# Optimization experiments

Measured on AMD Instinct MI355X. Metric: run time of the kernel, lower is better.

The kernel has to match this reference:

```python
import jax, jax.numpy as jnp
import numpy as np

N, D, E = 16384, 2048, 64   # tokens, d_model, num_experts
K = 9                        # self.k = min(k+1, num_experts) with k=8
EPS = 0.01
SIGMA = 1.0 / E              # Normal(0, 1/num_experts) stddev


def setup_inputs() -> dict:
    key = jax.random.key(0)
    ks = jax.random.split(key, 6)
    x = jax.random.normal(ks[0], (N, D), jnp.float32)
    Wr = jax.random.normal(ks[1], (D, E), jnp.float32) * 0.02
    br = jnp.zeros((E,), jnp.float32)
    Wn = jax.random.normal(ks[2], (D, E), jnp.float32) * 0.02
    bn = jnp.zeros((E,), jnp.float32)
    noise_eps = jax.random.normal(ks[3], (N, E), jnp.float32)
    # torch: (-empty.exponential_()).log() -> log of Exp(1) samples
    gumbel_noise = jnp.log(jax.random.exponential(ks[4], (N, E), jnp.float32))
    return {"x": x, "Wr": Wr, "br": br, "Wn": Wn, "bn": bn,
            "noise_eps": noise_eps, "gumbel_noise": gumbel_noise}


def reference(x, Wr, br, Wn, bn, noise_eps, gumbel_noise):
    raw_logits = x @ Wr + br                              # [N, E]
    noise_stddev = jax.nn.softplus(x @ Wn + bn) + EPS     # [N, E]
    noisy_logits = raw_logits + noise_eps * noise_stddev  # [N, E]

    top_vals, top_idx = jax.lax.top_k(noisy_logits, K)    # [N, K] sorted desc
    # scatter ones at top-k indices (indices unique per row)
    hard_mask = jax.nn.one_hot(top_idx, E, dtype=noisy_logits.dtype).sum(axis=1)  # [N, E]

    # gumbel-softmax straight-through relaxation
    mask_soft = jax.nn.softmax(noisy_logits + gumbel_noise, axis=-1)
    expert_mask = hard_mask - jax.lax.stop_gradient(mask_soft) + mask_soft

    route_prob = jax.nn.softmax(noisy_logits, axis=-1)    # [N, E]
    importance = jax.nn.softmax(raw_logits, axis=-1).sum(axis=0)  # [E]

    # load: P(raw + noise > threshold), Normal(0, 1/E) CDF per original
    threshold = top_vals[:, K - 1]                        # [N]
    z = (threshold[:, None] - raw_logits) / noise_stddev  # [N, E]
    cdf = 0.5 * (1.0 + jax.scipy.special.erf(z / (SIGMA * jnp.sqrt(jnp.float32(2.0)))))
    load = (1.0 - cdf).sum(axis=0)                        # [E]

    return (expert_mask, route_prob, importance, load)
```

## Files before the change

### kernel.cpp

```cpp
#include <hip/hip_runtime.h>
#include <hip/hip_bf16.h>
#include <math.h>

#define N_TOK 16384
#define DIM   2048
#define NE    64
#define TOPK  9

#define ROWS     16
#define DC       64
#define NCHUNK   (DIM / DC)
#define NTHREADS 256
#define NBUF     4

typedef short  short8  __attribute__((ext_vector_type(8)));
typedef float  float4_ __attribute__((ext_vector_type(4)));
typedef unsigned short ushort_t;

__device__ __forceinline__ void async16(const void* g, void* l) {
    __builtin_amdgcn_global_load_lds(
        (const __attribute__((address_space(1))) void*)g,
        (__attribute__((address_space(3))) void*)l, 16, 0, 0);
}

__device__ __forceinline__ unsigned pk2(float a, float b) {
    float2 f; f.x = a; f.y = b;
    __hip_bfloat162 h = __float22bfloat162_rn(f);
    unsigned u;
    __builtin_memcpy(&u, &h, 4);
    return u;
}

__device__ __forceinline__ void cvt8(const float4_ va, const float4_ vb,
                                     short8* h, short8* l) {
    union { short8 s; unsigned u[4]; } H, L;
    const float f[8] = {va[0], va[1], va[2], va[3], vb[0], vb[1], vb[2], vb[3]};
#pragma unroll
    for (int i = 0; i < 4; ++i) {
        const float a = f[2 * i], b = f[2 * i + 1];
        const unsigned p = pk2(a, b);
        H.u[i] = p;
        const float ha = __uint_as_float(p << 16);
        const float hb = __uint_as_float(p & 0xffff0000u);
        L.u[i] = pk2(a - ha, b - hb);
    }
    *h = H.s; *l = L.s;
}

__device__ __forceinline__ void wave_max64_2(float& a, float& b) {
#pragma unroll
    for (int off = 32; off > 0; off >>= 1) {
        const float ax = __shfl_xor(a, off, 64);
        const float bx = __shfl_xor(b, off, 64);
        a = fmaxf(a, ax);
        b = fmaxf(b, bx);
    }
}

__device__ __forceinline__ void wave_sum64_3(float& a, float& b, float& c) {
#pragma unroll
    for (int off = 32; off > 0; off >>= 1) {
        const float ax = __shfl_xor(a, off, 64);
        const float bx = __shfl_xor(b, off, 64);
        const float cx = __shfl_xor(c, off, 64);
        a += ax;
        b += bx;
        c += cx;
    }
}

__global__ __launch_bounds__(256)
void prep_w(const float* __restrict__ Wr, const float* __restrict__ Wn,
            ushort_t* __restrict__ wsW)
{
    const int gid = blockIdx.x * 256 + threadIdx.x;
    const int l   = gid & 63;
    const int ct  = (gid >> 6) & 7;
    const int kcg = gid >> 9;
    const int n   = ct * 16 + (l & 15);
    const int k0  = kcg * 32 + (l >> 4) * 8;
    const float* src = (n < NE) ? (Wr + n) : (Wn + (n - NE));
    union { short8 s; ushort_t us[8]; } H, L;
#pragma unroll
    for (int j = 0; j < 8; ++j) {
        const float v = src[(size_t)(k0 + j) * NE];
        const unsigned uv = __float_as_uint(v);
        const unsigned hb = (uv + 0x7fffu + ((uv >> 16) & 1u)) & 0xffff0000u;
        const float lo = v - __uint_as_float(hb);
        const unsigned ul = __float_as_uint(lo);
        H.us[j] = (ushort_t)(hb >> 16);
        L.us[j] = (ushort_t)((ul + 0x7fffu + ((ul >> 16) & 1u)) >> 16);
    }
    const size_t s0 = (size_t)(kcg * 8 + ct) * 2;
    *(short8*)(wsW + s0 * 512 + l * 8)         = H.s;
    *(short8*)(wsW + (s0 + 1) * 512 + l * 8)   = L.s;
}

struct BFrag { short8 h[2][2]; short8 l[2][2]; };

__device__ __forceinline__ void load_b(const char* __restrict__ wsB,
                                       int ch, int w, int lane, BFrag& b) {
#pragma unroll
    for (int kc = 0; kc < 2; ++kc)
#pragma unroll
        for (int cc = 0; cc < 2; ++cc) {
            const size_t off = (size_t)(((ch * 2 + kc) * 8) + 2 * w + cc) * 2048
                             + (size_t)lane * 16;
            b.h[kc][cc] = *(const short8*)(wsB + off);
            b.l[kc][cc] = *(const short8*)(wsB + off + 1024);
        }
}

__device__ __forceinline__ void mfma_chunk(const float* __restrict__ xb,
                                           const int (&aoff)[2][2],
                                           const BFrag& b,
                                           float4_ (&acc)[2]) {
#pragma unroll
    for (int kc = 0; kc < 2; ++kc) {
        const float4_ va = *(const float4_*)(xb + aoff[kc][0]);
        const float4_ vb = *(const float4_*)(xb + aoff[kc][1]);
        short8 ah, al;
        cvt8(va, vb, &ah, &al);
#pragma unroll
        for (int cc = 0; cc < 2; ++cc) {
            acc[cc] = __builtin_amdgcn_mfma_f32_16x16x32_bf16(ah, b.h[kc][cc], acc[cc], 0, 0, 0);
            acc[cc] = __builtin_amdgcn_mfma_f32_16x16x32_bf16(al, b.h[kc][cc], acc[cc], 0, 0, 0);
            acc[cc] = __builtin_amdgcn_mfma_f32_16x16x32_bf16(ah, b.l[kc][cc], acc[cc], 0, 0, 0);
        }
    }
}

__global__ __launch_bounds__(NTHREADS, 4)
void moe_main(const float* __restrict__ x,
              const float* __restrict__ br,
              const float* __restrict__ bn,
              const float* __restrict__ noise_eps,
              const float* __restrict__ gumbel,
              const ushort_t* __restrict__ wsW,
              float* __restrict__ out)
{
    __shared__ __align__(16) float smem[4352];

    const int t    = threadIdx.x;
    const int lane = t & 63;
    const int w    = t >> 6;
    const int c4   = lane & 15;
    const int q    = lane >> 4;
    const int row0 = blockIdx.x * ROWS;

    const int  srow = 4 * w + q;
    const int  sgk  = c4 ^ (srow & 15);
    const float* gxb = x + (size_t)(row0 + srow) * DIM + sgk * 4;
    const int  lxo  = w * 256;

    int aoff[2][2];
#pragma unroll
    for (int kc = 0; kc < 2; ++kc) {
        const int g0 = kc * 8 + q * 2;
        aoff[kc][0] = c4 * 64 + ((g0 ^ c4) * 4);
        aoff[kc][1] = c4 * 64 + (((g0 + 1) ^ c4) * 4);
    }

    float4_ acc[2];
    acc[0] = (float4_)(0.f);
    acc[1] = (float4_)(0.f);

    const char* wsB = (const char*)wsW;

#pragma unroll
    for (int p = 0; p < NBUF - 1; ++p)
        async16(gxb + p * DC, &smem[p * 1024 + lxo]);

    BFrag bA, bB;
    load_b(wsB, 0, w, lane, bA);

#pragma unroll 1
    for (int i = 0; i < NCHUNK - 4; i += 2) {
        asm volatile("s_waitcnt vmcnt(10)" ::: "memory");
        __builtin_amdgcn_s_barrier();
        asm volatile("" ::: "memory");
        load_b(wsB, i + 1, w, lane, bB);
        async16(gxb + (i + 3) * DC, &smem[((i + 3) & 3) * 1024 + lxo]);
        __builtin_amdgcn_sched_barrier(0);
        mfma_chunk(&smem[(i & 3) * 1024], aoff, bA, acc);

        asm volatile("s_waitcnt vmcnt(10)" ::: "memory");
        __builtin_amdgcn_s_barrier();
        asm volatile("" ::: "memory");
        load_b(wsB, i + 2, w, lane, bA);
        async16(gxb + (i + 4) * DC, &smem[((i + 4) & 3) * 1024 + lxo]);
        __builtin_amdgcn_sched_barrier(0);
        mfma_chunk(&smem[((i + 1) & 3) * 1024], aoff, bB, acc);
    }

    asm volatile("s_waitcnt vmcnt(10)" ::: "memory");
    __builtin_amdgcn_s_barrier();
    asm volatile("" ::: "memory");
    load_b(wsB, 29, w, lane, bB);
    async16(gxb + 31 * DC, &smem[3 * 1024 + lxo]);
    __builtin_amdgcn_sched_barrier(0);
    mfma_chunk(&smem[0 * 1024], aoff, bA, acc);

    asm volatile("s_waitcnt vmcnt(10)" ::: "memory");
    __builtin_amdgcn_s_barrier();
    asm volatile("" ::: "memory");
    load_b(wsB, 30, w, lane, bA);
    __builtin_amdgcn_sched_barrier(0);
    mfma_chunk(&smem[1 * 1024], aoff, bB, acc);

    asm volatile("s_waitcnt vmcnt(9)" ::: "memory");
    __builtin_amdgcn_s_barrier();
    asm volatile("" ::: "memory");
    load_b(wsB, 31, w, lane, bB);
    __builtin_amdgcn_sched_barrier(0);
    mfma_chunk(&smem[2 * 1024], aoff, bA, acc);

    asm volatile("s_waitcnt vmcnt(8)" ::: "memory");
    __builtin_amdgcn_s_barrier();
    asm volatile("" ::: "memory");
    __builtin_amdgcn_sched_barrier(0);
    mfma_chunk(&smem[3 * 1024], aoff, bB, acc);

    float epsv[4], gumv[4];
#pragma unroll
    for (int r = 0; r < 4; ++r) {
        const int row = row0 + w * 4 + r;
        epsv[r] = noise_eps[(size_t)row * NE + lane];
        gumv[r] = gumbel  [(size_t)row * NE + lane];
    }

    __syncthreads();
    float* rawS = &smem[0];
    float* noiS = &smem[2080];
#pragma unroll
    for (int cc = 0; cc < 2; ++cc) {
        const int colg = (2 * w + cc) * 16 + c4;
        float* basep = (colg < NE) ? rawS : noiS;
        const int col = colg & 63;
#pragma unroll
        for (int v = 0; v < 4; ++v) {
            const int row = q * 4 + v;
            basep[row * 65 + col] = acc[cc][v];
        }
    }
    __syncthreads();

    const float br_l = br[lane];
    const float bn_l = bn[lane];

    float imp_acc = 0.f, load_acc = 0.f;
    float* out_em   = out;
    float* out_rp   = out + (size_t)N_TOK * NE;
    float* out_imp  = out + (size_t)2 * N_TOK * NE;
    float* out_load = out_imp + NE;

#pragma unroll 1
    for (int r = 0; r < 4; ++r) {
        const int lrow = w * 4 + r;
        const int row  = row0 + lrow;
        const float raw = rawS[lrow * 65 + lane] + br_l;
        const float nl  = noiS[lrow * 65 + lane] + bn_l;
        const float sd = fmaxf(nl, 0.f) + log1pf(expf(-fabsf(nl))) + 0.01f;
        const float noisy = fmaf(epsv[r], sd, raw);

        const unsigned uk  = __float_as_uint(noisy);
        const unsigned key = uk ^ ((uk & 0x80000000u) ? 0xFFFFFFFFu : 0x80000000u);
        unsigned res = 0;
#pragma unroll
        for (int bit = 31; bit >= 0; --bit) {
            const unsigned cand = res | (1u << bit);
            const int cnt = __popcll(__ballot(key >= cand));
            if (cnt >= TOPK) res = cand;
        }
        const float thr  = __uint_as_float(res ^ ((res & 0x80000000u) ? 0x80000000u : 0xFFFFFFFFu));
        const float hard = (key >= res) ? 1.f : 0.f;

        const float g = noisy + gumv[r];
        float mg = g, mr = raw;
        wave_max64_2(mg, mr);

        const float eg = expf(g - mg);
        const float en = expf(noisy - thr);
        const float er = expf(raw - mr);
        float sg = eg, sn = en, sr = er;
        wave_sum64_3(sg, sn, sr);

        const float ms = eg / sg;
        const float em = (hard - ms) + ms;
        const float rp = en / sn;
        imp_acc += er / sr;

        const float z = (thr - raw) / sd;
        load_acc += 0.5f * erfcf(z * 45.254833995939045f);

        out_em[(size_t)row * NE + lane] = em;
        out_rp[(size_t)row * NE + lane] = rp;
    }

    __syncthreads();
    smem[w * 64 + lane]       = imp_acc;
    smem[256 + w * 64 + lane] = load_acc;
    __syncthreads();
    if (w == 0) {
        const float s1 = smem[lane] + smem[64 + lane] + smem[128 + lane] + smem[192 + lane];
        const float s2 = smem[256 + lane] + smem[320 + lane] + smem[384 + lane] + smem[448 + lane];
        atomicAdd(&out_imp[lane], s1);
        atomicAdd(&out_load[lane], s2);
    }
}

extern "C" void kernel_launch(void* const* d_in, const int* in_sizes, int n_in,
                              void* d_out, int out_size, void* d_ws, size_t ws_size,
                              hipStream_t stream)
{
    const float* x         = (const float*)d_in[0];
    const float* Wr        = (const float*)d_in[1];
    const float* br        = (const float*)d_in[2];
    const float* Wn        = (const float*)d_in[3];
    const float* bn        = (const float*)d_in[4];
    const float* noise_eps = (const float*)d_in[5];
    const float* gumbel    = (const float*)d_in[6];
    float* out = (float*)d_out;
    ushort_t* wsW = (ushort_t*)d_ws;

    (void)hipMemsetAsync((char*)d_out + (size_t)2 * N_TOK * NE * sizeof(float), 0,
                         2 * NE * sizeof(float), stream);
    prep_w<<<128, 256, 0, stream>>>(Wr, Wn, wsW);
    moe_main<<<N_TOK / ROWS, NTHREADS, 0, stream>>>(
        x, br, bn, noise_eps, gumbel, wsW, out);
}
```

Before: 261.2 us.

## Restructure GEMM main loop into uniform pipelined steps with 8 LDS buffers

The prologue, steady-state loop and epilogue of the x-tile pipeline are replaced by a templated step that issues the next weight-fragment loads and the async x load before waiting and computing. LDS reads now go through inline-asm ds_read_b128 with an explicit lgkmcnt wait. The LDS ring grows from 4 to 8 buffers and vmcnt thresholds are raised, so more global loads can be in flight before the barrier. Tail steps clamp the chunk indices and issue redundant loads instead of having a special epilogue. The larger shared-memory footprint could reduce occupancy, and the extra tail loads add some memory traffic.

```diff
diff --git a/kernel.cpp b/kernel.cpp
--- a/kernel.cpp
+++ b/kernel.cpp
@@ -11,7 +11,7 @@
 #define DC       64
 #define NCHUNK   (DIM / DC)
 #define NTHREADS 256
-#define NBUF     4
+#define NBUF     8
 
 typedef short  short8  __attribute__((ext_vector_type(8)));
 typedef float  float4_ __attribute__((ext_vector_type(4)));
@@ -21,6 +21,12 @@
     __builtin_amdgcn_global_load_lds(
         (const __attribute__((address_space(1))) void*)g,
         (__attribute__((address_space(3))) void*)l, 16, 0, 0);
+}
+
+__device__ __forceinline__ float4_ ds_read128(unsigned addr) {
+    float4_ d;
+    asm volatile("ds_read_b128 %0, %1" : "=v"(d) : "v"(addr));
+    return d;
 }
 
 __device__ __forceinline__ unsigned pk2(float a, float b) {
@@ -111,23 +117,58 @@
         }
 }
 
-__device__ __forceinline__ void mfma_chunk(const float* __restrict__ xb,
-                                           const int (&aoff)[2][2],
-                                           const BFrag& b,
-                                           float4_ (&acc)[2]) {
-#pragma unroll
-    for (int kc = 0; kc < 2; ++kc) {
-        const float4_ va = *(const float4_*)(xb + aoff[kc][0]);
-        const float4_ vb = *(const float4_*)(xb + aoff[kc][1]);
-        short8 ah, al;
-        cvt8(va, vb, &ah, &al);
-#pragma unroll
-        for (int cc = 0; cc < 2; ++cc) {
-            acc[cc] = __builtin_amdgcn_mfma_f32_16x16x32_bf16(ah, b.h[kc][cc], acc[cc], 0, 0, 0);
-            acc[cc] = __builtin_amdgcn_mfma_f32_16x16x32_bf16(al, b.h[kc][cc], acc[cc], 0, 0, 0);
-            acc[cc] = __builtin_amdgcn_mfma_f32_16x16x32_bf16(ah, b.l[kc][cc], acc[cc], 0, 0, 0);
-        }
-    }
+template<int W>
+__device__ __forceinline__ void wait_vm() {
+    static_assert(W == 11 || W == 19 || W == 27, "unexpected wait");
+    if constexpr (W == 11)      asm volatile("s_waitcnt vmcnt(11)" ::: "memory");
+    else if constexpr (W == 19) asm volatile("s_waitcnt vmcnt(19)" ::: "memory");
+    else                        asm volatile("s_waitcnt vmcnt(27)" ::: "memory");
+}
+
+__device__ __forceinline__ void compute_chunk(unsigned ldsb,
+                                              const unsigned (&aoffB)[2][2],
+                                              const BFrag& b,
+                                              float4_ (&acc)[2]) {
+    const float4_ va0 = ds_read128(ldsb + aoffB[0][0]);
+    const float4_ vb0 = ds_read128(ldsb + aoffB[0][1]);
+    const float4_ va1 = ds_read128(ldsb + aoffB[1][0]);
+    const float4_ vb1 = ds_read128(ldsb + aoffB[1][1]);
+    asm volatile("s_waitcnt lgkmcnt(0)" ::: "memory");
+    __builtin_amdgcn_sched_barrier(0);
+    short8 ah0, al0, ah1, al1;
+    cvt8(va0, vb0, &ah0, &al0);
+    cvt8(va1, vb1, &ah1, &al1);
+#pragma unroll
+    for (int cc = 0; cc < 2; ++cc) {
+        acc[cc] = __builtin_amdgcn_mfma_f32_16x16x32_bf16(ah0, b.h[0][cc], acc[cc], 0, 0, 0);
+        acc[cc] = __builtin_amdgcn_mfma_f32_16x16x32_bf16(al0, b.h[0][cc], acc[cc], 0, 0, 0);
+        acc[cc] = __builtin_amdgcn_mfma_f32_16x16x32_bf16(ah0, b.l[0][cc], acc[cc], 0, 0, 0);
+    }
+#pragma unroll
+    for (int cc = 0; cc < 2; ++cc) {
+        acc[cc] = __builtin_amdgcn_mfma_f32_16x16x32_bf16(ah1, b.h[1][cc], acc[cc], 0, 0, 0);
+        acc[cc] = __builtin_amdgcn_mfma_f32_16x16x32_bf16(al1, b.h[1][cc], acc[cc], 0, 0, 0);
+        acc[cc] = __builtin_amdgcn_mfma_f32_16x16x32_bf16(ah1, b.l[1][cc], acc[cc], 0, 0, 0);
+    }
+}
+
+template<int W>
+__device__ __forceinline__ void step(int i, const char* wsB, int w, int lane,
+                                     BFrag& bload, const BFrag& buse,
+                                     const float* gxb, float* smem, int lxo,
+                                     unsigned ldsbase, const unsigned (&aoffB)[2][2],
+                                     float4_ (&acc)[2])
+{
+    const int bch = (i + 1 < NCHUNK) ? i + 1 : NCHUNK - 1;
+    load_b(wsB, bch, w, lane, bload);
+    __builtin_amdgcn_sched_barrier(0);
+    const int sch = (i + 3 < NCHUNK) ? i + 3 : NCHUNK - 1;
+    async16(gxb + sch * DC, &smem[((i + 3) & (NBUF - 1)) * 1024 + lxo]);
+    __builtin_amdgcn_sched_barrier(0);
+    wait_vm<W>();
+    __builtin_amdgcn_s_barrier();
+    __builtin_amdgcn_sched_barrier(0);
+    compute_chunk(ldsbase + (unsigned)((i & (NBUF - 1)) * 4096), aoffB, buse, acc);
 }
 
 __global__ __launch_bounds__(NTHREADS, 4)
@@ -139,7 +180,7 @@
               const ushort_t* __restrict__ wsW,
               float* __restrict__ out)
 {
-    __shared__ __align__(16) float smem[4352];
+    __shared__ __align__(16) float smem[NBUF * 1024];
 
     const int t    = threadIdx.x;
     const int lane = t & 63;
@@ -153,13 +194,15 @@
     const float* gxb = x + (size_t)(row0 + srow) * DIM + sgk * 4;
     const int  lxo  = w * 256;
 
-    int aoff[2][2];
+    unsigned aoffB[2][2];
 #pragma unroll
     for (int kc = 0; kc < 2; ++kc) {
         const int g0 = kc * 8 + q * 2;
-        aoff[kc][0] = c4 * 64 + ((g0 ^ c4) * 4);
-        aoff[kc][1] = c4 * 64 + (((g0 + 1) ^ c4) * 4);
-    }
+        aoffB[kc][0] = (unsigned)((c4 * 64 + ((g0 ^ c4) * 4)) * 4);
+        aoffB[kc][1] = (unsigned)((c4 * 64 + (((g0 + 1) ^ c4) * 4)) * 4);
+    }
+    const unsigned ldsbase =
+        (unsigned)(unsigned long long)(__attribute__((address_space(3))) void*)(void*)smem;
 
     float4_ acc[2];
     acc[0] = (float4_)(0.f);
@@ -167,59 +210,23 @@
 
     const char* wsB = (const char*)wsW;
 
-#pragma unroll
-    for (int p = 0; p < NBUF - 1; ++p)
-        async16(gxb + p * DC, &smem[p * 1024 + lxo]);
-
     BFrag bA, bB;
     load_b(wsB, 0, w, lane, bA);
-
+    __builtin_amdgcn_sched_barrier(0);
+    async16(gxb + 0 * DC, &smem[0 * 1024 + lxo]);
+    __builtin_amdgcn_sched_barrier(0);
+    async16(gxb + 1 * DC, &smem[1 * 1024 + lxo]);
+    __builtin_amdgcn_sched_barrier(0);
+    async16(gxb + 2 * DC, &smem[2 * 1024 + lxo]);
+    __builtin_amdgcn_sched_barrier(0);
+
+    step<11>(0, wsB, w, lane, bB, bA, gxb, smem, lxo, ldsbase, aoffB, acc);
+    step<19>(1, wsB, w, lane, bA, bB, gxb, smem, lxo, ldsbase, aoffB, acc);
 #pragma unroll 1
-    for (int i = 0; i < NCHUNK - 4; i += 2) {
-        asm volatile("s_waitcnt vmcnt(10)" ::: "memory");
-        __builtin_amdgcn_s_barrier();
-        asm volatile("" ::: "memory");
-        load_b(wsB, i + 1, w, lane, bB);
-        async16(gxb + (i + 3) * DC, &smem[((i + 3) & 3) * 1024 + lxo]);
-        __builtin_amdgcn_sched_barrier(0);
-        mfma_chunk(&smem[(i & 3) * 1024], aoff, bA, acc);
-
-        asm volatile("s_waitcnt vmcnt(10)" ::: "memory");
-        __builtin_amdgcn_s_barrier();
-        asm volatile("" ::: "memory");
-        load_b(wsB, i + 2, w, lane, bA);
-        async16(gxb + (i + 4) * DC, &smem[((i + 4) & 3) * 1024 + lxo]);
-        __builtin_amdgcn_sched_barrier(0);
-        mfma_chunk(&smem[((i + 1) & 3) * 1024], aoff, bB, acc);
-    }
-
-    asm volatile("s_waitcnt vmcnt(10)" ::: "memory");
-    __builtin_amdgcn_s_barrier();
-    asm volatile("" ::: "memory");
-    load_b(wsB, 29, w, lane, bB);
-    async16(gxb + 31 * DC, &smem[3 * 1024 + lxo]);
-    __builtin_amdgcn_sched_barrier(0);
-    mfma_chunk(&smem[0 * 1024], aoff, bA, acc);
-
-    asm volatile("s_waitcnt vmcnt(10)" ::: "memory");
-    __builtin_amdgcn_s_barrier();
-    asm volatile("" ::: "memory");
-    load_b(wsB, 30, w, lane, bA);
-    __builtin_amdgcn_sched_barrier(0);
-    mfma_chunk(&smem[1 * 1024], aoff, bB, acc);
-
-    asm volatile("s_waitcnt vmcnt(9)" ::: "memory");
-    __builtin_amdgcn_s_barrier();
-    asm volatile("" ::: "memory");
-    load_b(wsB, 31, w, lane, bB);
-    __builtin_amdgcn_sched_barrier(0);
-    mfma_chunk(&smem[2 * 1024], aoff, bA, acc);
-
-    asm volatile("s_waitcnt vmcnt(8)" ::: "memory");
-    __builtin_amdgcn_s_barrier();
-    asm volatile("" ::: "memory");
-    __builtin_amdgcn_sched_barrier(0);
-    mfma_chunk(&smem[3 * 1024], aoff, bB, acc);
+    for (int i = 2; i < NCHUNK; i += 2) {
+        step<27>(i,     wsB, w, lane, bB, bA, gxb, smem, lxo, ldsbase, aoffB, acc);
+        step<27>(i + 1, wsB, w, lane, bA, bB, gxb, smem, lxo, ldsbase, aoffB, acc);
+    }
 
     float epsv[4], gumv[4];
 #pragma unroll
```

After: 260.8 us. No clear change (-0.1%).
